# Kernel optimization log

Hardware: AMD Instinct MI355X
Metric: run time of the kernel (lower is better)

Reference implementation:

```python
import jax, jax.numpy as jnp
import numpy as np

B, S, D = 4, 2048, 1024  # batch, seq_len, d_model (d_in == d_model)


def setup_inputs() -> dict:
    key = jax.random.key(0)
    ks = jax.random.split(key, 9)
    scale = 1.0 / np.sqrt(D)
    return {
        "q": jax.random.normal(ks[0], (B, S, D), jnp.float32),
        "k": jax.random.normal(ks[1], (B, S, D), jnp.float32),
        "v": jax.random.normal(ks[2], (B, S, D), jnp.float32),
        "Wq": jax.random.normal(ks[3], (D, D), jnp.float32) * scale,
        "bq": jnp.zeros((D,), jnp.float32),
        "Wk": jax.random.normal(ks[4], (D, D), jnp.float32) * scale,
        "bk": jnp.zeros((D,), jnp.float32),
        "Wv": jax.random.normal(ks[5], (D, D), jnp.float32) * scale,
        "bv": jnp.zeros((D,), jnp.float32),
    }


def reference(q, k, v, Wq, bq, Wk, bk, Wv, bv):
    query = q @ Wq + bq                      # [B, S, D]
    key_p = k @ Wk + bk                      # [B, S, D]
    value = v @ Wv + bv                      # [B, S, D]
    inv_sqrt_d = 1.0 / jnp.sqrt(jnp.asarray(D, query.dtype))
    scores = jnp.einsum('bqd,bkd->bqk', query, key_p) * inv_sqrt_d  # [B, S, S]
    w = jax.nn.softmax(scores, axis=-1)
    return jnp.einsum('bqk,bkd->bqd', w, value)  # [B, S, D]
```

## Files before the change

kernel.cpp:

```cpp
#include <hip/hip_runtime.h>
#include <math.h>


using short8  = __attribute__((ext_vector_type(8))) short;
using floatx4 = __attribute__((ext_vector_type(4))) float;

__device__ __forceinline__ unsigned short f2bf(float f) {
    union { float f; unsigned u; } x; x.f = f;
    return (unsigned short)((x.u + 0x8000u) >> 16);
}

__device__ __forceinline__ void gload_lds16(const unsigned short* g, unsigned short* l) {
    __builtin_amdgcn_global_load_lds(
        (const __attribute__((address_space(1))) unsigned int*)g,
        (__attribute__((address_space(3))) unsigned int*)l, 16, 0, 0);
}

#define SBAR    __builtin_amdgcn_s_barrier()
#define SCHEDB  __builtin_amdgcn_sched_barrier(0)
#define LGKM(n) asm volatile("s_waitcnt lgkmcnt(" #n ")" ::: "memory")
#define VMW(n)  asm volatile("s_waitcnt vmcnt(" #n ")" ::: "memory")

__global__ __launch_bounds__(256) void prep(
    const float* __restrict__ q, const float* __restrict__ k, const float* __restrict__ v,
    const float* __restrict__ W0, const float* __restrict__ W1, const float* __restrict__ W2,
    unsigned short* __restrict__ qkvbf, unsigned short* __restrict__ Wt)
{
    __shared__ float tile[32][33];
    const int id = blockIdx.x;
    const int t  = threadIdx.x;
    if (id < 24576) {
        const int z  = id >> 13;
        const int xb = id & 8191;
        const float* x = (z == 0) ? q : (z == 1) ? k : v;
        const size_t i = ((size_t)xb * 256 + t) * 4;
        const float4 a = *(const float4*)(x + i);
        ushort4 p = { f2bf(a.x), f2bf(a.y), f2bf(a.z), f2bf(a.w) };
        *(ushort4*)(qkvbf + (size_t)z * 8192 * 1024 + i) = p;
    } else {
        const int idt = id - 24576;
        const int z  = idt >> 10;
        const int r  = idt & 1023;
        const int bx = (r & 31) * 32;
        const int by = (r >> 5) * 32;
        const float* W = (z == 0) ? W0 : (z == 1) ? W1 : W2;
        unsigned short* o = Wt + (size_t)z * 1024 * 1024;
        const int tx = t & 31;
        const int ty = (t >> 5) * 4;
        #pragma unroll
        for (int rr = 0; rr < 4; ++rr)
            tile[ty + rr][tx] = W[(size_t)(by + ty + rr) * 1024 + bx + tx];
        __syncthreads();
        #pragma unroll
        for (int rr = 0; rr < 4; ++rr)
            o[(size_t)(bx + ty + rr) * 1024 + by + tx] = f2bf(tile[tx][ty + rr]);
    }
}


#define STAGE_A(bb, kh, tt) do { \
    gload_lds16(gA + (size_t)srowA * lda + (tt) * 64 + (kh) * 32 + scol, \
                lds + (bb) * 24576 + (kh) * 4096 + t512 * 8); \
} while (0)

#define STAGE_B(bb, kh, tt) do { \
    const unsigned short* s_ = gB + (size_t)srowA * ldb + (tt) * 64 + (kh) * 32 + scol; \
    unsigned short* d_ = lds + (bb) * 24576 + 8192 + (kh) * 8192 + t512 * 8; \
    gload_lds16(s_, d_); \
    gload_lds16(s_ + (size_t)128 * ldb, d_ + 4096); \
} while (0)

#define LDSA(bb, kh, i) (*(const short8*)&lds[(bb) * 24576 + (kh) * 4096 + (arow + (i) * 16) * 32 + rslot])
#define LDSB(bb, kh, j) (*(const short8*)&lds[(bb) * 24576 + 8192 + (kh) * 8192 + (brow + (j) * 16) * 32 + rslot])

#define READ8(dA, dB, bb, kh) do { \
    _Pragma("unroll") \
    for (int j_ = 0; j_ < 4; ++j_) dB[j_] = LDSB(bb, kh, j_); \
    _Pragma("unroll") \
    for (int i_ = 0; i_ < 4; ++i_) dA[i_] = LDSA(bb, kh, i_); \
} while (0)

#define MFMA16(Af, Bf) do { \
    __builtin_amdgcn_s_setprio(1); \
    _Pragma("unroll") \
    for (int i_ = 0; i_ < 4; ++i_) \
        _Pragma("unroll") \
        for (int j_ = 0; j_ < 4; ++j_) \
            acc[i_][j_] = __builtin_amdgcn_mfma_f32_16x16x32_bf16( \
                Af[i_], Bf[j_], acc[i_][j_], 0, 0, 0); \
    __builtin_amdgcn_s_setprio(0); \
} while (0)

__device__ __forceinline__ void gemm_pipe(
    const unsigned short* __restrict__ gA, int lda,
    const unsigned short* __restrict__ gB, int ldb,
    int nt, unsigned short* lds, floatx4 (&acc)[4][4])
{
    const int t512 = threadIdx.x;
    const int lane = t512 & 63;
    const int wave = t512 >> 6;
    const int wr   = wave >> 2;
    const int wc   = wave & 3;
    const int l15  = lane & 15;
    const int quad = lane >> 4;
    const int srowA = t512 >> 2;
    const int scol  = ((t512 & 3) ^ ((t512 >> 3) & 3)) * 8;
    const int rslot = (quad ^ ((l15 >> 1) & 3)) * 8;
    const int arow  = wr * 64 + l15;
    const int brow  = wc * 64 + l15;

    short8 cA[4], cB[4], nA[4], nB[4];

    STAGE_A(0, 0, 0); STAGE_B(0, 0, 0);
    STAGE_A(0, 1, 0); STAGE_B(0, 1, 0);
    STAGE_A(1, 0, 1); STAGE_B(1, 0, 1);
    STAGE_A(1, 1, 1); STAGE_B(1, 1, 1);
    VMW(9);
    SBAR;
    READ8(cA, cB, 0, 0);
    VMW(6);
    SBAR;

    int b0 = 0, b1 = 1, b2 = 2;
    for (int t = 0; t < nt; ++t) {
        READ8(nA, nB, b0, 1);
        if (t + 2 < nt) { STAGE_A(b2, 0, t + 2); STAGE_B(b2, 0, t + 2); }
        LGKM(8); SCHEDB;
        MFMA16(cA, cB);
        if (t + 1 < nt) {
            if (t + 2 < nt) { VMW(6); } else { VMW(3); }
            SBAR;
            READ8(cA, cB, b1, 0);
            if (t + 2 < nt) { STAGE_A(b2, 1, t + 2); STAGE_B(b2, 1, t + 2); }
            LGKM(8); SCHEDB;
            MFMA16(nA, nB);
            if (t + 2 < nt) { VMW(6); } else { VMW(0); }
            SBAR;
        } else {
            LGKM(0); SCHEDB;
            MFMA16(nA, nB);
        }
        const int tmp = b0; b0 = b1; b1 = b2; b2 = tmp;
    }
}

#define EPI_IDS                                   \
    const int tt   = threadIdx.x;                 \
    const int lane = tt & 63;                     \
    const int wave = tt >> 6;                     \
    const int wr   = wave >> 2;                   \
    const int wc   = wave & 3;                    \
    const int l15  = lane & 15;                   \
    const int quad = lane >> 4;

__global__ __launch_bounds__(512) void proj8(
    const unsigned short* __restrict__ Abf,
    const unsigned short* __restrict__ Wt,
    const float* __restrict__ bq, const float* __restrict__ bk, const float* __restrict__ bv,
    unsigned short* __restrict__ Qp, unsigned short* __restrict__ Kp,
    unsigned short* __restrict__ Vpt)
{
    __shared__ __attribute__((aligned(16))) unsigned short lds[73728];
    const int id = blockIdx.x;
    const int g  = (id & 7) * 96 + (id >> 3);
    const int z  = g >> 8;
    const int r  = g & 255;
    const int m0 = (r >> 2) * 128;
    const int n0 = (r & 3) * 256;

    const unsigned short* gA = Abf + (size_t)z * 8192 * 1024 + (size_t)m0 * 1024;
    const unsigned short* gB = Wt  + (size_t)z * 1024 * 1024 + (size_t)n0 * 1024;

    floatx4 acc[4][4] = {};
    gemm_pipe(gA, 1024, gB, 1024, 16, lds, acc);

    EPI_IDS
    const float* bias = (z == 0) ? bq : (z == 1) ? bk : bv;
    #pragma unroll
    for (int j = 0; j < 4; ++j) {
        const int col = n0 + wc * 64 + j * 16 + l15;
        const float bv_ = bias[col];
        #pragma unroll
        for (int i = 0; i < 4; ++i) {
            const int row = m0 + wr * 64 + i * 16 + quad * 4;
            if (z < 2) {
                unsigned short* C = (z == 0) ? Qp : Kp;
                #pragma unroll
                for (int r2 = 0; r2 < 4; ++r2)
                    C[(size_t)(row + r2) * 1024 + col] = f2bf(acc[i][j][r2] + bv_);
            } else {
                ushort4 p = { f2bf(acc[i][j][0] + bv_), f2bf(acc[i][j][1] + bv_),
                              f2bf(acc[i][j][2] + bv_), f2bf(acc[i][j][3] + bv_) };
                *(ushort4*)&Vpt[(size_t)col * 8192 + row] = p;
            }
        }
    }
}

__global__ __launch_bounds__(512) void scores8(
    const unsigned short* __restrict__ Qp,
    const unsigned short* __restrict__ Kp,
    unsigned short* __restrict__ Pexp,
    float* __restrict__ rowsum)
{
    __shared__ __attribute__((aligned(16))) unsigned short lds[73728];
    const int id = blockIdx.x;
    const int g  = (id & 7) * 64 + (id >> 3);
    const int z  = g >> 7;
    const int r  = g & 127;
    const int m0 = (r >> 3) * 128;
    const int n0 = (r & 7) * 256;

    const unsigned short* gA = Qp + (size_t)z * 2048 * 1024 + (size_t)m0 * 1024;
    const unsigned short* gB = Kp + (size_t)z * 2048 * 1024 + (size_t)n0 * 1024;

    floatx4 acc[4][4] = {};
    gemm_pipe(gA, 1024, gB, 1024, 16, lds, acc);

    EPI_IDS
    unsigned short* P = Pexp + (size_t)z * 2048 * 2048;
    float* rs = rowsum + (size_t)z * 2048;
    #pragma unroll
    for (int i = 0; i < 4; ++i) {
        const int rowb = m0 + wr * 64 + i * 16 + quad * 4;
        float sm[4] = {0.f, 0.f, 0.f, 0.f};
        #pragma unroll
        for (int j = 0; j < 4; ++j) {
            const int col = n0 + wc * 64 + j * 16 + l15;
            #pragma unroll
            for (int r2 = 0; r2 < 4; ++r2) {
                const float p = __expf(acc[i][j][r2] * 0.03125f);
                sm[r2] += p;
                P[(size_t)(rowb + r2) * 2048 + col] = f2bf(p);
            }
        }
        #pragma unroll
        for (int r2 = 0; r2 < 4; ++r2) {
            float s = sm[r2];
            s += __shfl_xor(s, 1);
            s += __shfl_xor(s, 2);
            s += __shfl_xor(s, 4);
            s += __shfl_xor(s, 8);
            if (l15 == 0)
                atomicAdd(&rs[rowb + r2], s);
        }
    }
}

__global__ __launch_bounds__(512) void pv8(
    const unsigned short* __restrict__ Pexp,
    const unsigned short* __restrict__ Vpt,
    const float* __restrict__ rowsum,
    float* __restrict__ out)
{
    __shared__ __attribute__((aligned(16))) unsigned short lds[73728];
    const int id = blockIdx.x;
    const int g  = (id & 7) * 32 + (id >> 3);
    const int z  = g >> 6;
    const int r  = g & 63;
    const int m0 = (r >> 2) * 128;
    const int n0 = (r & 3) * 256;

    const unsigned short* gA = Pexp + (size_t)z * 2048 * 2048 + (size_t)m0 * 2048;
    const unsigned short* gB = Vpt  + (size_t)n0 * 8192 + (size_t)z * 2048;

    floatx4 acc[4][4] = {};
    gemm_pipe(gA, 2048, gB, 8192, 32, lds, acc);

    EPI_IDS
    const float* rs = rowsum + (size_t)z * 2048;
    float* C = out + (size_t)z * 2048 * 1024;
    #pragma unroll
    for (int i = 0; i < 4; ++i) {
        const int rowb = m0 + wr * 64 + i * 16 + quad * 4;
        float inv[4];
        #pragma unroll
        for (int r2 = 0; r2 < 4; ++r2) inv[r2] = 1.0f / rs[rowb + r2];
        #pragma unroll
        for (int j = 0; j < 4; ++j) {
            const int col = n0 + wc * 64 + j * 16 + l15;
            #pragma unroll
            for (int r2 = 0; r2 < 4; ++r2)
                C[(size_t)(rowb + r2) * 1024 + col] = acc[i][j][r2] * inv[r2];
        }
    }
}

extern "C" void kernel_launch(void* const* d_in, const int* in_sizes, int n_in,
                              void* d_out, int out_size, void* d_ws, size_t ws_size,
                              hipStream_t stream)
{
    const float* q  = (const float*)d_in[0];
    const float* k  = (const float*)d_in[1];
    const float* v  = (const float*)d_in[2];
    const float* Wq = (const float*)d_in[3];
    const float* bq = (const float*)d_in[4];
    const float* Wk = (const float*)d_in[5];
    const float* bk = (const float*)d_in[6];
    const float* Wv = (const float*)d_in[7];
    const float* bv = (const float*)d_in[8];
    float* out = (float*)d_out;

    const int Bn = 4, S = 2048;

    char* w = (char*)d_ws;
    unsigned short* Wt     = (unsigned short*)(w);
    unsigned short* Qp     = (unsigned short*)(w + (6u << 20));
    unsigned short* Kp     = (unsigned short*)(w + (22u << 20));
    unsigned short* Vpt    = (unsigned short*)(w + (38u << 20));
    unsigned short* qkvbf  = (unsigned short*)(w + (54u << 20));
    unsigned short* Pexp   = (unsigned short*)(w + (54u << 20));
    float*          rowsum = (float*)(w + (86u << 20));

    hipMemsetAsync(rowsum, 0, (size_t)Bn * S * sizeof(float), stream);

    prep<<<dim3(27648), dim3(256), 0, stream>>>(q, k, v, Wq, Wk, Wv, qkvbf, Wt);

    proj8<<<dim3(768), dim3(512), 0, stream>>>(qkvbf, Wt, bq, bk, bv, Qp, Kp, Vpt);

    scores8<<<dim3(512), dim3(512), 0, stream>>>(Qp, Kp, Pexp, rowsum);

    pv8<<<dim3(256), dim3(512), 0, stream>>>(Pexp, Vpt, rowsum, out);
}
```

Baseline: 303.2 us.

## Restructure GEMM pipeline to 4-wave blocks with triple-buffered K=32 stages

Replaces the 8-wave 128x256 GEMM core with a 4-wave variant where each wave computes a 128x64 tile (8x4 MFMA accumulators) over K-steps of 32. It uses a 3-deep LDS ring with one barrier per step and a simpler prefetch schedule. LDS use per block is halved and launch bounds now allow two blocks per CU. The aim is to raise occupancy and reduce barrier and sync overhead, at the cost of more registers per wave and no register double-buffering of fragments.

```diff
diff --git a/kernel.cpp b/kernel.cpp
--- a/kernel.cpp
+++ b/kernel.cpp
@@ -58,109 +58,86 @@
 }
 
 
-#define STAGE_A(bb, kh, tt) do { \
-    gload_lds16(gA + (size_t)srowA * lda + (tt) * 64 + (kh) * 32 + scol, \
-                lds + (bb) * 24576 + (kh) * 4096 + t512 * 8); \
+#define STAGE(bb, tt) do { \
+    _Pragma("unroll") \
+    for (int p_ = 0; p_ < 2; ++p_) \
+        gload_lds16(gA + (size_t)(p_ * 64 + srowA) * lda + (tt) * 32 + scol, \
+                    lds + (bb) * 12288 + p_ * 2048 + t256 * 8); \
+    _Pragma("unroll") \
+    for (int p_ = 0; p_ < 4; ++p_) \
+        gload_lds16(gB + (size_t)(p_ * 64 + srowA) * ldb + (tt) * 32 + scol, \
+                    lds + (bb) * 12288 + 4096 + p_ * 2048 + t256 * 8); \
 } while (0)
 
-#define STAGE_B(bb, kh, tt) do { \
-    const unsigned short* s_ = gB + (size_t)srowA * ldb + (tt) * 64 + (kh) * 32 + scol; \
-    unsigned short* d_ = lds + (bb) * 24576 + 8192 + (kh) * 8192 + t512 * 8; \
-    gload_lds16(s_, d_); \
-    gload_lds16(s_ + (size_t)128 * ldb, d_ + 4096); \
-} while (0)
-
-#define LDSA(bb, kh, i) (*(const short8*)&lds[(bb) * 24576 + (kh) * 4096 + (arow + (i) * 16) * 32 + rslot])
-#define LDSB(bb, kh, j) (*(const short8*)&lds[(bb) * 24576 + 8192 + (kh) * 8192 + (brow + (j) * 16) * 32 + rslot])
-
-#define READ8(dA, dB, bb, kh) do { \
-    _Pragma("unroll") \
-    for (int j_ = 0; j_ < 4; ++j_) dB[j_] = LDSB(bb, kh, j_); \
-    _Pragma("unroll") \
-    for (int i_ = 0; i_ < 4; ++i_) dA[i_] = LDSA(bb, kh, i_); \
-} while (0)
-
-#define MFMA16(Af, Bf) do { \
+#define LDSA(bb, i) (*(const short8*)&lds[(bb) * 12288 + ((i) * 16 + l15) * 32 + rslot])
+#define LDSB(bb, j) (*(const short8*)&lds[(bb) * 12288 + 4096 + (wv * 64 + (j) * 16 + l15) * 32 + rslot])
+
+#define MFMA32 do { \
     __builtin_amdgcn_s_setprio(1); \
     _Pragma("unroll") \
-    for (int i_ = 0; i_ < 4; ++i_) \
+    for (int i_ = 0; i_ < 8; ++i_) \
         _Pragma("unroll") \
         for (int j_ = 0; j_ < 4; ++j_) \
             acc[i_][j_] = __builtin_amdgcn_mfma_f32_16x16x32_bf16( \
-                Af[i_], Bf[j_], acc[i_][j_], 0, 0, 0); \
+                af[i_], bf[j_], acc[i_][j_], 0, 0, 0); \
     __builtin_amdgcn_s_setprio(0); \
 } while (0)
 
-__device__ __forceinline__ void gemm_pipe(
+__device__ __forceinline__ void gemm_w4(
     const unsigned short* __restrict__ gA, int lda,
     const unsigned short* __restrict__ gB, int ldb,
-    int nt, unsigned short* lds, floatx4 (&acc)[4][4])
-{
-    const int t512 = threadIdx.x;
-    const int lane = t512 & 63;
-    const int wave = t512 >> 6;
-    const int wr   = wave >> 2;
-    const int wc   = wave & 3;
+    int nt, unsigned short* lds, floatx4 (&acc)[8][4])
+{
+    const int t256 = threadIdx.x;
+    const int lane = t256 & 63;
+    const int wv   = t256 >> 6;
     const int l15  = lane & 15;
     const int quad = lane >> 4;
-    const int srowA = t512 >> 2;
-    const int scol  = ((t512 & 3) ^ ((t512 >> 3) & 3)) * 8;
+    const int srowA = t256 >> 2;
+    const int scol  = ((t256 & 3) ^ ((t256 >> 3) & 3)) * 8;
     const int rslot = (quad ^ ((l15 >> 1) & 3)) * 8;
-    const int arow  = wr * 64 + l15;
-    const int brow  = wc * 64 + l15;
-
-    short8 cA[4], cB[4], nA[4], nB[4];
-
-    STAGE_A(0, 0, 0); STAGE_B(0, 0, 0);
-    STAGE_A(0, 1, 0); STAGE_B(0, 1, 0);
-    STAGE_A(1, 0, 1); STAGE_B(1, 0, 1);
-    STAGE_A(1, 1, 1); STAGE_B(1, 1, 1);
-    VMW(9);
-    SBAR;
-    READ8(cA, cB, 0, 0);
-    VMW(6);
+
+    short8 af[8], bf[4];
+
+    STAGE(0, 0); STAGE(1, 1); STAGE(2, 2);
+    VMW(12);
     SBAR;
 
     int b0 = 0, b1 = 1, b2 = 2;
     for (int t = 0; t < nt; ++t) {
-        READ8(nA, nB, b0, 1);
-        if (t + 2 < nt) { STAGE_A(b2, 0, t + 2); STAGE_B(b2, 0, t + 2); }
-        LGKM(8); SCHEDB;
-        MFMA16(cA, cB);
+        #pragma unroll
+        for (int j = 0; j < 4; ++j) bf[j] = LDSB(b0, j);
+        #pragma unroll
+        for (int i = 0; i < 8; ++i) af[i] = LDSA(b0, i);
+        LGKM(0); SCHEDB;
+        SBAR;
+        if (t + 3 < nt) STAGE(b0, t + 3);
+        MFMA32;
         if (t + 1 < nt) {
-            if (t + 2 < nt) { VMW(6); } else { VMW(3); }
+            if (t + 3 < nt)      { VMW(12); }
+            else if (t + 2 < nt) { VMW(6);  }
+            else                 { VMW(0);  }
             SBAR;
-            READ8(cA, cB, b1, 0);
-            if (t + 2 < nt) { STAGE_A(b2, 1, t + 2); STAGE_B(b2, 1, t + 2); }
-            LGKM(8); SCHEDB;
-            MFMA16(nA, nB);
-            if (t + 2 < nt) { VMW(6); } else { VMW(0); }
-            SBAR;
-        } else {
-            LGKM(0); SCHEDB;
-            MFMA16(nA, nB);
-        }
-        const int tmp = b0; b0 = b1; b1 = b2; b2 = tmp;
+            const int tmp = b0; b0 = b1; b1 = b2; b2 = tmp;
+        }
     }
 }
 
 #define EPI_IDS                                   \
     const int tt   = threadIdx.x;                 \
     const int lane = tt & 63;                     \
-    const int wave = tt >> 6;                     \
-    const int wr   = wave >> 2;                   \
-    const int wc   = wave & 3;                    \
+    const int wv   = tt >> 6;                     \
     const int l15  = lane & 15;                   \
     const int quad = lane >> 4;
 
-__global__ __launch_bounds__(512) void proj8(
+__global__ __launch_bounds__(256, 2) void proj8(
     const unsigned short* __restrict__ Abf,
     const unsigned short* __restrict__ Wt,
     const float* __restrict__ bq, const float* __restrict__ bk, const float* __restrict__ bv,
     unsigned short* __restrict__ Qp, unsigned short* __restrict__ Kp,
     unsigned short* __restrict__ Vpt)
 {
-    __shared__ __attribute__((aligned(16))) unsigned short lds[73728];
+    __shared__ __attribute__((aligned(16))) unsigned short lds[36864];
     const int id = blockIdx.x;
     const int g  = (id & 7) * 96 + (id >> 3);
     const int z  = g >> 8;
@@ -171,18 +148,18 @@
     const unsigned short* gA = Abf + (size_t)z * 8192 * 1024 + (size_t)m0 * 1024;
     const unsigned short* gB = Wt  + (size_t)z * 1024 * 1024 + (size_t)n0 * 1024;
 
-    floatx4 acc[4][4] = {};
-    gemm_pipe(gA, 1024, gB, 1024, 16, lds, acc);
+    floatx4 acc[8][4] = {};
+    gemm_w4(gA, 1024, gB, 1024, 32, lds, acc);
 
     EPI_IDS
     const float* bias = (z == 0) ? bq : (z == 1) ? bk : bv;
     #pragma unroll
     for (int j = 0; j < 4; ++j) {
-        const int col = n0 + wc * 64 + j * 16 + l15;
+        const int col = n0 + wv * 64 + j * 16 + l15;
         const float bv_ = bias[col];
         #pragma unroll
-        for (int i = 0; i < 4; ++i) {
-            const int row = m0 + wr * 64 + i * 16 + quad * 4;
+        for (int i = 0; i < 8; ++i) {
+            const int row = m0 + i * 16 + quad * 4;
             if (z < 2) {
                 unsigned short* C = (z == 0) ? Qp : Kp;
                 #pragma unroll
@@ -197,13 +174,13 @@
     }
 }
 
-__global__ __launch_bounds__(512) void scores8(
+__global__ __launch_bounds__(256, 2) void scores8(
     const unsigned short* __restrict__ Qp,
     const unsigned short* __restrict__ Kp,
     unsigned short* __restrict__ Pexp,
     float* __restrict__ rowsum)
 {
-    __shared__ __attribute__((aligned(16))) unsigned short lds[73728];
+    __shared__ __attribute__((aligned(16))) unsigned short lds[36864];
     const int id = blockIdx.x;
     const int g  = (id & 7) * 64 + (id >> 3);
     const int z  = g >> 7;
@@ -214,19 +191,19 @@
     const unsigned short* gA = Qp + (size_t)z * 2048 * 1024 + (size_t)m0 * 1024;
     const unsigned short* gB = Kp + (size_t)z * 2048 * 1024 + (size_t)n0 * 1024;
 
-    floatx4 acc[4][4] = {};
-    gemm_pipe(gA, 1024, gB, 1024, 16, lds, acc);
+    floatx4 acc[8][4] = {};
+    gemm_w4(gA, 1024, gB, 1024, 32, lds, acc);
 
     EPI_IDS
     unsigned short* P = Pexp + (size_t)z * 2048 * 2048;
     float* rs = rowsum + (size_t)z * 2048;
     #pragma unroll
-    for (int i = 0; i < 4; ++i) {
-        const int rowb = m0 + wr * 64 + i * 16 + quad * 4;
+    for (int i = 0; i < 8; ++i) {
+        const int rowb = m0 + i * 16 + quad * 4;
         float sm[4] = {0.f, 0.f, 0.f, 0.f};
         #pragma unroll
         for (int j = 0; j < 4; ++j) {
-            const int col = n0 + wc * 64 + j * 16 + l15;
+            const int col = n0 + wv * 64 + j * 16 + l15;
             #pragma unroll
             for (int r2 = 0; r2 < 4; ++r2) {
                 const float p = __expf(acc[i][j][r2] * 0.03125f);
@@ -247,13 +224,13 @@
     }
 }
 
-__global__ __launch_bounds__(512) void pv8(
+__global__ __launch_bounds__(256, 2) void pv8(
     const unsigned short* __restrict__ Pexp,
     const unsigned short* __restrict__ Vpt,
     const float* __restrict__ rowsum,
     float* __restrict__ out)
 {
-    __shared__ __attribute__((aligned(16))) unsigned short lds[73728];
+    __shared__ __attribute__((aligned(16))) unsigned short lds[36864];
     const int id = blockIdx.x;
     const int g  = (id & 7) * 32 + (id >> 3);
     const int z  = g >> 6;
@@ -264,21 +241,21 @@
     const unsigned short* gA = Pexp + (size_t)z * 2048 * 2048 + (size_t)m0 * 2048;
     const unsigned short* gB = Vpt  + (size_t)n0 * 8192 + (size_t)z * 2048;
 
-    floatx4 acc[4][4] = {};
-    gemm_pipe(gA, 2048, gB, 8192, 32, lds, acc);
+    floatx4 acc[8][4] = {};
+    gemm_w4(gA, 2048, gB, 8192, 64, lds, acc);
 
     EPI_IDS
     const float* rs = rowsum + (size_t)z * 2048;
     float* C = out + (size_t)z * 2048 * 1024;
     #pragma unroll
-    for (int i = 0; i < 4; ++i) {
-        const int rowb = m0 + wr * 64 + i * 16 + quad * 4;
+    for (int i = 0; i < 8; ++i) {
+        const int rowb = m0 + i * 16 + quad * 4;
         float inv[4];
         #pragma unroll
         for (int r2 = 0; r2 < 4; ++r2) inv[r2] = 1.0f / rs[rowb + r2];
         #pragma unroll
         for (int j = 0; j < 4; ++j) {
-            const int col = n0 + wc * 64 + j * 16 + l15;
+            const int col = n0 + wv * 64 + j * 16 + l15;
             #pragma unroll
             for (int r2 = 0; r2 < 4; ++r2)
                 C[(size_t)(rowb + r2) * 1024 + col] = acc[i][j][r2] * inv[r2];
@@ -316,9 +293,9 @@
 
     prep<<<dim3(27648), dim3(256), 0, stream>>>(q, k, v, Wq, Wk, Wv, qkvbf, Wt);
 
-    proj8<<<dim3(768), dim3(512), 0, stream>>>(qkvbf, Wt, bq, bk, bv, Qp, Kp, Vpt);
-
-    scores8<<<dim3(512), dim3(512), 0, stream>>>(Qp, Kp, Pexp, rowsum);
-
-    pv8<<<dim3(256), dim3(512), 0, stream>>>(Pexp, Vpt, rowsum, out);
-}
+    proj8<<<dim3(768), dim3(256), 0, stream>>>(qkvbf, Wt, bq, bk, bv, Qp, Kp, Vpt);
+
+    scores8<<<dim3(512), dim3(256), 0, stream>>>(Qp, Kp, Pexp, rowsum);
+
+    pv8<<<dim3(256), dim3(256), 0, stream>>>(Pexp, Vpt, rowsum, out);
+}
```

Measured after the change: 306.8 us. Within noise of the previous version (+1.2%).
